# Kernel tuning notes

Measured on AMD Instinct MI355X. Metric: run time of the kernel, lower is better.

Reference implementation:

```python
import jax, jax.numpy as jnp
import numpy as np
from jax import lax

WINDOW_SIZE = 11
SIGMA = 1.5
CHANNELS = 3
C1 = 0.01 ** 2
C2 = 0.03 ** 2


def _create_window():
    coords = jnp.arange(WINDOW_SIZE, dtype=jnp.float32) - WINDOW_SIZE // 2
    g = jnp.exp(-coords ** 2 / (2.0 * SIGMA ** 2))
    g = g / g.sum()
    w2d = g[:, None] * g[None, :]                      # (11, 11)
    # depthwise kernel, OIHW with groups=channels -> (C, 1, k, k)
    return jnp.broadcast_to(w2d, (CHANNELS, 1, WINDOW_SIZE, WINDOW_SIZE))


def _dwconv(x, window):
    pad = WINDOW_SIZE // 2
    return lax.conv_general_dilated(
        x, window,
        window_strides=(1, 1),
        padding=[(pad, pad), (pad, pad)],
        dimension_numbers=('NCHW', 'OIHW', 'NCHW'),
        feature_group_count=CHANNELS,
    )


def setup_inputs() -> dict:
    key = jax.random.key(0)
    k1, k2 = jax.random.split(key)
    pred = jax.random.uniform(k1, (32, 3, 512, 512), dtype=jnp.float32)
    target = jax.random.uniform(k2, (32, 3, 512, 512), dtype=jnp.float32)
    return {"pred": pred, "target": target}


def reference(pred, target):
    pred = pred.astype(jnp.float32)
    target = target.astype(jnp.float32)
    window = _create_window()

    mu1 = _dwconv(pred, window)
    mu2 = _dwconv(target, window)
    mu1_sq = mu1 * mu1
    mu2_sq = mu2 * mu2
    mu1_mu2 = mu1 * mu2
    sigma1_sq = _dwconv(pred * pred, window) - mu1_sq
    sigma2_sq = _dwconv(target * target, window) - mu2_sq
    sigma12 = _dwconv(pred * target, window) - mu1_mu2

    ssim_map = ((2.0 * mu1_mu2 + C1) * (2.0 * sigma12 + C2)) / (
        (mu1_sq + mu2_sq + C1) * (sigma1_sq + sigma2_sq + C2))
    return 1.0 - ssim_map.mean()
```

## Files before the change

kernel.cpp:

```cpp
#include <hip/hip_runtime.h>
#include <hip/hip_bf16.h>
#include <math.h>

#define BLOCK 256
#define IMG 512
#define CHUNK 128
#define NSTEP 9
#define RSTR 40
#define NBLOCKS 3072
#define NACC 128
#define N_TOTAL 25165824.0f

typedef float f32x4 __attribute__((ext_vector_type(4)));
typedef short s16x8 __attribute__((ext_vector_type(8)));

struct WB { unsigned short b[11]; float corr; };
union FR { unsigned int u[4]; s16x8 s; };

__device__ __forceinline__ unsigned int pk2(float a, float b) {
    union { __hip_bfloat162 h; unsigned int u; } cv;
    cv.h = __float22bfloat162_rn(make_float2(a, b));
    return cv.u;
}

__global__ __launch_bounds__(BLOCK, 5)
void ssim_stream(const float* __restrict__ pred,
                 const float* __restrict__ targ,
                 float* __restrict__ accum, WB wb) {
    __shared__ unsigned short s_w[3][16][32];
    __shared__ unsigned short s_ring[4][5][16][RSTR];

    const int tid = threadIdx.x;
    for (int e = tid; e < 3 * 512; e += BLOCK) {
        const int mat = e >> 9;
        const int m   = (e >> 5) & 15;
        const int k   = e & 31;
        int idx;
        if (mat == 0) idx = k - m - 3;
        else          idx = (k - m - (mat == 2 ? 16 : 0)) & 31;
        s_w[mat][m][k] = (idx >= 0 && idx <= 10) ? wb.b[idx] : (unsigned short)0;
    }
    __syncthreads();

    const int wave = tid >> 6;
    const int lane = tid & 63;
    const int l15  = lane & 15;
    const int quad = lane >> 4;

    const int S     = blockIdx.x * 4 + wave;
    const int plane = S >> 7;
    const int rem   = S & 127;
    const int C0    = (rem >> 2) * 16;
    const int R0    = (rem & 3) * CHUNK;

    const float* P = pred + (size_t)plane * (IMG * IMG);
    const float* T = targ + (size_t)plane * (IMG * IMG);

    FR bw;  bw.s  = *(const s16x8*)&s_w[0][l15][quad * 8];
    FR aw0; aw0.s = *(const s16x8*)&s_w[1][l15][quad * 8];
    FR aw1; aw1.s = *(const s16x8*)&s_w[2][l15][quad * 8];

    unsigned short (*ring)[16][RSTR] = s_ring[wave];

    const int  cb    = C0 - 8 + 8 * quad;
    const bool colok = (cb >= 0) && (cb <= IMG - 8);
    const float corr = wb.corr;
    const float C1v = 0.0001f, C2v = 0.0009f;
    const f32x4 z = {0.f, 0.f, 0.f, 0.f};
    float lsum = 0.f;

    float xc[8], yc[8];
    {
        const int gr = R0 - 5 + l15;
        const bool ok = colok && (gr >= 0) && (gr < IMG);
        if (ok) {
            const float* rp = P + ((size_t)gr << 9) + cb;
            const float* tp = T + ((size_t)gr << 9) + cb;
            float4 a0 = *(const float4*)rp, a1 = *(const float4*)(rp + 4);
            float4 b0 = *(const float4*)tp, b1 = *(const float4*)(tp + 4);
            xc[0]=a0.x; xc[1]=a0.y; xc[2]=a0.z; xc[3]=a0.w;
            xc[4]=a1.x; xc[5]=a1.y; xc[6]=a1.z; xc[7]=a1.w;
            yc[0]=b0.x; yc[1]=b0.y; yc[2]=b0.z; yc[3]=b0.w;
            yc[4]=b1.x; yc[5]=b1.y; yc[6]=b1.z; yc[7]=b1.w;
        } else {
#pragma unroll
            for (int i = 0; i < 8; ++i) { xc[i] = 0.f; yc[i] = 0.f; }
        }
    }

    for (int s = 0; s < NSTEP; ++s) {
        float xn[8], yn[8];
        const bool have_next = (s + 1 < NSTEP);
        if (have_next) {
            const int gr = R0 - 5 + 16 * (s + 1) + l15;
            const bool ok = colok && (gr >= 0) && (gr < IMG);
            if (ok) {
                const float* rp = P + ((size_t)gr << 9) + cb;
                const float* tp = T + ((size_t)gr << 9) + cb;
                float4 a0 = *(const float4*)rp, a1 = *(const float4*)(rp + 4);
                float4 b0 = *(const float4*)tp, b1 = *(const float4*)(tp + 4);
                xn[0]=a0.x; xn[1]=a0.y; xn[2]=a0.z; xn[3]=a0.w;
                xn[4]=a1.x; xn[5]=a1.y; xn[6]=a1.z; xn[7]=a1.w;
                yn[0]=b0.x; yn[1]=b0.y; yn[2]=b0.z; yn[3]=b0.w;
                yn[4]=b1.x; yn[5]=b1.y; yn[6]=b1.z; yn[7]=b1.w;
            } else {
#pragma unroll
                for (int i = 0; i < 8; ++i) { xn[i] = 0.f; yn[i] = 0.f; }
            }
        } else {
#pragma unroll
            for (int i = 0; i < 8; ++i) { xn[i] = 0.f; yn[i] = 0.f; }
        }

        FR ax, ay, axx, ayy, axy;
#pragma unroll
        for (int p = 0; p < 4; ++p) {
            const float xa = xc[2*p], xb = xc[2*p+1];
            const float ya = yc[2*p], yb = yc[2*p+1];
            ax.u[p]  = pk2(xa, xb);
            ay.u[p]  = pk2(ya, yb);
            axx.u[p] = pk2(xa * xa, xb * xb);
            ayy.u[p] = pk2(ya * ya, yb * yb);
            axy.u[p] = pk2(xa * ya, xb * yb);
        }
        f32x4 d0 = __builtin_amdgcn_mfma_f32_16x16x32_bf16(ax.s,  bw.s, z, 0, 0, 0);
        f32x4 d1 = __builtin_amdgcn_mfma_f32_16x16x32_bf16(ay.s,  bw.s, z, 0, 0, 0);
        f32x4 d2 = __builtin_amdgcn_mfma_f32_16x16x32_bf16(axx.s, bw.s, z, 0, 0, 0);
        f32x4 d3 = __builtin_amdgcn_mfma_f32_16x16x32_bf16(ayy.s, bw.s, z, 0, 0, 0);
        f32x4 d4 = __builtin_amdgcn_mfma_f32_16x16x32_bf16(axy.s, bw.s, z, 0, 0, 0);

        const int pb = (16 * s + 4 * quad) & 31;
        *(uint2*)&ring[0][l15][pb] = make_uint2(pk2(d0[0], d0[1]), pk2(d0[2], d0[3]));
        *(uint2*)&ring[1][l15][pb] = make_uint2(pk2(d1[0], d1[1]), pk2(d1[2], d1[3]));
        *(uint2*)&ring[2][l15][pb] = make_uint2(pk2(d2[0], d2[1]), pk2(d2[2], d2[3]));
        *(uint2*)&ring[3][l15][pb] = make_uint2(pk2(d3[0], d3[1]), pk2(d3[2], d3[3]));
        *(uint2*)&ring[4][l15][pb] = make_uint2(pk2(d4[0], d4[1]), pk2(d4[2], d4[3]));

        if (s >= 1) {
            const int t = s - 1;
            const FR aw = (t & 1) ? aw1 : aw0;
            f32x4 acc[5];
#pragma unroll
            for (int q = 0; q < 5; ++q) {
                FR b; b.s = *(const s16x8*)&ring[q][l15][quad * 8];
                acc[q] = __builtin_amdgcn_mfma_f32_16x16x32_bf16(aw.s, b.s, z, 0, 0, 0);
            }
#pragma unroll
            for (int i = 0; i < 4; ++i) {
                const float mu1 = acc[0][i] * corr;
                const float mu2 = acc[1][i] * corr;
                const float exx = acc[2][i] * corr;
                const float eyy = acc[3][i] * corr;
                const float exy = acc[4][i] * corr;
                const float mu1s = mu1 * mu1;
                const float mu2s = mu2 * mu2;
                const float mu12 = mu1 * mu2;
                const float sg1  = exx - mu1s;
                const float sg2  = eyy - mu2s;
                const float sg12 = exy - mu12;
                const float num  = fmaf(2.f, mu12, C1v) * fmaf(2.f, sg12, C2v);
                const float den  = (mu1s + mu2s + C1v) * (sg1 + sg2 + C2v);
                lsum = fmaf(num, __builtin_amdgcn_rcpf(den), lsum);
            }
        }

#pragma unroll
        for (int i = 0; i < 8; ++i) { xc[i] = xn[i]; yc[i] = yn[i]; }
    }

#pragma unroll
    for (int off = 32; off > 0; off >>= 1) lsum += __shfl_down(lsum, off, 64);
    if (lane == 0) atomicAdd(&accum[S & (NACC - 1)], lsum);
}

__global__ void ssim_finalize(const float* __restrict__ accum, float* __restrict__ out) {
    const int l = threadIdx.x;
    float v = accum[l] + accum[l + 64];
#pragma unroll
    for (int off = 32; off > 0; off >>= 1) v += __shfl_down(v, off, 64);
    if (l == 0) out[0] = 1.0f - v * (1.0f / N_TOTAL);
}

extern "C" void kernel_launch(void* const* d_in, const int* in_sizes, int n_in,
                              void* d_out, int out_size, void* d_ws, size_t ws_size,
                              hipStream_t stream) {
    const float* pred = (const float*)d_in[0];
    const float* targ = (const float*)d_in[1];
    float* out = (float*)d_out;
    float* ws  = (float*)d_ws;

    WB wb;
    {
        double gg[11], sum = 0.0;
        for (int k = 0; k < 11; ++k) {
            const double d = (double)(k - 5);
            gg[k] = exp(-d * d / 4.5);
            sum += gg[k];
        }
        double sbf = 0.0;
        for (int k = 0; k < 11; ++k) {
            union { float f; unsigned int u; } cv;
            cv.f = (float)(gg[k] / sum);
            const unsigned int r = (cv.u + 0x7fffu + ((cv.u >> 16) & 1u)) >> 16;
            wb.b[k] = (unsigned short)r;
            union { float f; unsigned int u; } bk;
            bk.u = r << 16;
            sbf += (double)bk.f;
        }
        wb.corr = (float)(1.0 / (sbf * sbf));
    }

    hipMemsetAsync(ws, 0, NACC * sizeof(float), stream);
    ssim_stream<<<NBLOCKS, BLOCK, 0, stream>>>(pred, targ, ws, wb);
    ssim_finalize<<<1, 64, 0, stream>>>(ws, out);
}
```

Measured before the change: 273.5 us.

## Share horizontal halo across waves via block-wide bf16 staging tile

Each block now cooperatively loads an 80-column strip of both images, converts the five products to bf16 in shared memory, and lets four waves each compute a 16-column output slice from it. This removes the redundant halo loads and conversions each wave previously did on its own 32-column window. In exchange it adds two block barriers per row step, more shared memory, and lowers the occupancy hint from 5 to 3 blocks.

```diff
diff --git a/kernel.cpp b/kernel.cpp
--- a/kernel.cpp
+++ b/kernel.cpp
@@ -4,8 +4,7 @@
 
 #define BLOCK 256
 #define IMG 512
-#define CHUNK 128
-#define NSTEP 9
+#define SW 84
 #define RSTR 40
 #define NBLOCKS 3072
 #define NACC 128
@@ -23,12 +22,22 @@
     return cv.u;
 }
 
-__global__ __launch_bounds__(BLOCK, 5)
-void ssim_stream(const float* __restrict__ pred,
-                 const float* __restrict__ targ,
-                 float* __restrict__ accum, WB wb) {
+__device__ __forceinline__ void stage5(unsigned short (*sq)[16][SW],
+                                       int r, int i, float4 xv, float4 yv) {
+    *(uint2*)&sq[0][r][4*i] = make_uint2(pk2(xv.x,xv.y), pk2(xv.z,xv.w));
+    *(uint2*)&sq[1][r][4*i] = make_uint2(pk2(yv.x,yv.y), pk2(yv.z,yv.w));
+    *(uint2*)&sq[2][r][4*i] = make_uint2(pk2(xv.x*xv.x,xv.y*xv.y), pk2(xv.z*xv.z,xv.w*xv.w));
+    *(uint2*)&sq[3][r][4*i] = make_uint2(pk2(yv.x*yv.x,yv.y*yv.y), pk2(yv.z*yv.z,yv.w*yv.w));
+    *(uint2*)&sq[4][r][4*i] = make_uint2(pk2(xv.x*yv.x,xv.y*yv.y), pk2(xv.z*yv.z,xv.w*yv.w));
+}
+
+__global__ __launch_bounds__(BLOCK, 3)
+void ssim_tiled(const float* __restrict__ pred,
+                const float* __restrict__ targ,
+                float* __restrict__ accum, WB wb) {
     __shared__ unsigned short s_w[3][16][32];
-    __shared__ unsigned short s_ring[4][5][16][RSTR];
+    __shared__ unsigned short s_q[5][16][SW];
+    __shared__ unsigned short s_ring[5][64][RSTR];
 
     const int tid = threadIdx.x;
     for (int e = tid; e < 3 * 512; e += BLOCK) {
@@ -40,101 +49,97 @@
         else          idx = (k - m - (mat == 2 ? 16 : 0)) & 31;
         s_w[mat][m][k] = (idx >= 0 && idx <= 10) ? wb.b[idx] : (unsigned short)0;
     }
-    __syncthreads();
-
-    const int wave = tid >> 6;
+
+    const int bx    = blockIdx.x;
+    const int plane = bx >> 5;
+    const int rem   = bx & 31;
+    const int tx    = rem >> 2;
+    const int ry    = rem & 3;
+    const int C0    = tx * 64;
+    const int R0    = ry * 128;
+
+    const float* P = pred + (size_t)plane * (IMG * IMG);
+    const float* T = targ + (size_t)plane * (IMG * IMG);
+
+    const int w    = tid >> 6;
     const int lane = tid & 63;
     const int l15  = lane & 15;
     const int quad = lane >> 4;
 
-    const int S     = blockIdx.x * 4 + wave;
-    const int plane = S >> 7;
-    const int rem   = S & 127;
-    const int C0    = (rem >> 2) * 16;
-    const int R0    = (rem & 3) * CHUNK;
-
-    const float* P = pred + (size_t)plane * (IMG * IMG);
-    const float* T = targ + (size_t)plane * (IMG * IMG);
-
-    FR bw;  bw.s  = *(const s16x8*)&s_w[0][l15][quad * 8];
-    FR aw0; aw0.s = *(const s16x8*)&s_w[1][l15][quad * 8];
-    FR aw1; aw1.s = *(const s16x8*)&s_w[2][l15][quad * 8];
-
-    unsigned short (*ring)[16][RSTR] = s_ring[wave];
-
-    const int  cb    = C0 - 8 + 8 * quad;
-    const bool colok = (cb >= 0) && (cb <= IMG - 8);
+    const int slotA = w * 80 + lane;
+    const int rA = slotA / 20, iA = slotA % 20;
+    const int colA = C0 - 8 + 4 * iA;
+    const bool okcA = (colA >= 0) && (colA + 4 <= IMG);
+    const bool hasB = (lane < 16);
+    const int slotB = w * 80 + 64 + l15;
+    const int rB = slotB / 20, iB = slotB % 20;
+    const int colB = C0 - 8 + 4 * iB;
+    const bool okcB = (colB >= 0) && (colB + 4 <= IMG);
+
     const float corr = wb.corr;
     const float C1v = 0.0001f, C2v = 0.0009f;
     const f32x4 z = {0.f, 0.f, 0.f, 0.f};
     float lsum = 0.f;
 
-    float xc[8], yc[8];
+    float4 xA, yA, xB, yB;
     {
-        const int gr = R0 - 5 + l15;
-        const bool ok = colok && (gr >= 0) && (gr < IMG);
-        if (ok) {
-            const float* rp = P + ((size_t)gr << 9) + cb;
-            const float* tp = T + ((size_t)gr << 9) + cb;
-            float4 a0 = *(const float4*)rp, a1 = *(const float4*)(rp + 4);
-            float4 b0 = *(const float4*)tp, b1 = *(const float4*)(tp + 4);
-            xc[0]=a0.x; xc[1]=a0.y; xc[2]=a0.z; xc[3]=a0.w;
-            xc[4]=a1.x; xc[5]=a1.y; xc[6]=a1.z; xc[7]=a1.w;
-            yc[0]=b0.x; yc[1]=b0.y; yc[2]=b0.z; yc[3]=b0.w;
-            yc[4]=b1.x; yc[5]=b1.y; yc[6]=b1.z; yc[7]=b1.w;
-        } else {
-#pragma unroll
-            for (int i = 0; i < 8; ++i) { xc[i] = 0.f; yc[i] = 0.f; }
-        }
-    }
-
-    for (int s = 0; s < NSTEP; ++s) {
-        float xn[8], yn[8];
-        const bool have_next = (s + 1 < NSTEP);
-        if (have_next) {
-            const int gr = R0 - 5 + 16 * (s + 1) + l15;
-            const bool ok = colok && (gr >= 0) && (gr < IMG);
-            if (ok) {
-                const float* rp = P + ((size_t)gr << 9) + cb;
-                const float* tp = T + ((size_t)gr << 9) + cb;
-                float4 a0 = *(const float4*)rp, a1 = *(const float4*)(rp + 4);
-                float4 b0 = *(const float4*)tp, b1 = *(const float4*)(tp + 4);
-                xn[0]=a0.x; xn[1]=a0.y; xn[2]=a0.z; xn[3]=a0.w;
-                xn[4]=a1.x; xn[5]=a1.y; xn[6]=a1.z; xn[7]=a1.w;
-                yn[0]=b0.x; yn[1]=b0.y; yn[2]=b0.z; yn[3]=b0.w;
-                yn[4]=b1.x; yn[5]=b1.y; yn[6]=b1.z; yn[7]=b1.w;
-            } else {
-#pragma unroll
-                for (int i = 0; i < 8; ++i) { xn[i] = 0.f; yn[i] = 0.f; }
-            }
-        } else {
-#pragma unroll
-            for (int i = 0; i < 8; ++i) { xn[i] = 0.f; yn[i] = 0.f; }
-        }
-
-        FR ax, ay, axx, ayy, axy;
-#pragma unroll
-        for (int p = 0; p < 4; ++p) {
-            const float xa = xc[2*p], xb = xc[2*p+1];
-            const float ya = yc[2*p], yb = yc[2*p+1];
-            ax.u[p]  = pk2(xa, xb);
-            ay.u[p]  = pk2(ya, yb);
-            axx.u[p] = pk2(xa * xa, xb * xb);
-            ayy.u[p] = pk2(ya * ya, yb * yb);
-            axy.u[p] = pk2(xa * ya, xb * yb);
-        }
-        f32x4 d0 = __builtin_amdgcn_mfma_f32_16x16x32_bf16(ax.s,  bw.s, z, 0, 0, 0);
-        f32x4 d1 = __builtin_amdgcn_mfma_f32_16x16x32_bf16(ay.s,  bw.s, z, 0, 0, 0);
-        f32x4 d2 = __builtin_amdgcn_mfma_f32_16x16x32_bf16(axx.s, bw.s, z, 0, 0, 0);
-        f32x4 d3 = __builtin_amdgcn_mfma_f32_16x16x32_bf16(ayy.s, bw.s, z, 0, 0, 0);
-        f32x4 d4 = __builtin_amdgcn_mfma_f32_16x16x32_bf16(axy.s, bw.s, z, 0, 0, 0);
-
-        const int pb = (16 * s + 4 * quad) & 31;
-        *(uint2*)&ring[0][l15][pb] = make_uint2(pk2(d0[0], d0[1]), pk2(d0[2], d0[3]));
-        *(uint2*)&ring[1][l15][pb] = make_uint2(pk2(d1[0], d1[1]), pk2(d1[2], d1[3]));
-        *(uint2*)&ring[2][l15][pb] = make_uint2(pk2(d2[0], d2[1]), pk2(d2[2], d2[3]));
-        *(uint2*)&ring[3][l15][pb] = make_uint2(pk2(d3[0], d3[1]), pk2(d3[2], d3[3]));
-        *(uint2*)&ring[4][l15][pb] = make_uint2(pk2(d4[0], d4[1]), pk2(d4[2], d4[3]));
+        const int gr = R0 - 5 + rA;
+        if (okcA && gr >= 0) {
+            xA = *(const float4*)(P + ((size_t)gr << 9) + colA);
+            yA = *(const float4*)(T + ((size_t)gr << 9) + colA);
+        } else { xA = make_float4(0,0,0,0); yA = make_float4(0,0,0,0); }
+        const int grB = R0 - 5 + rB;
+        if (hasB && okcB && grB >= 0) {
+            xB = *(const float4*)(P + ((size_t)grB << 9) + colB);
+            yB = *(const float4*)(T + ((size_t)grB << 9) + colB);
+        } else { xB = make_float4(0,0,0,0); yB = make_float4(0,0,0,0); }
+    }
+    __syncthreads();
+
+    FR bw;  bw.s  = *(const s16x8*)&s_w[0][l15][quad * 8];
+    FR aw0; aw0.s = *(const s16x8*)&s_w[1][l15][quad * 8];
+    FR aw1; aw1.s = *(const s16x8*)&s_w[2][l15][quad * 8];
+
+    stage5(s_q, rA, iA, xA, yA);
+    if (hasB) stage5(s_q, rB, iB, xB, yB);
+    __syncthreads();
+
+    const int rcol = 16 * w + l15;
+
+    for (int s = 0; s < 9; ++s) {
+        float4 nxA, nyA, nxB, nyB;
+        if (s < 8) {
+            const int gr = R0 - 5 + 16 * (s + 1) + rA;
+            if (okcA && gr < IMG) {
+                nxA = *(const float4*)(P + ((size_t)gr << 9) + colA);
+                nyA = *(const float4*)(T + ((size_t)gr << 9) + colA);
+            } else { nxA = make_float4(0,0,0,0); nyA = make_float4(0,0,0,0); }
+            const int grB = R0 - 5 + 16 * (s + 1) + rB;
+            if (hasB && okcB && grB < IMG) {
+                nxB = *(const float4*)(P + ((size_t)grB << 9) + colB);
+                nyB = *(const float4*)(T + ((size_t)grB << 9) + colB);
+            } else { nxB = make_float4(0,0,0,0); nyB = make_float4(0,0,0,0); }
+        }
+
+        {
+            FR a0, a1, a2, a3, a4;
+            a0.s = *(const s16x8*)&s_q[0][l15][16*w + 8*quad];
+            a1.s = *(const s16x8*)&s_q[1][l15][16*w + 8*quad];
+            a2.s = *(const s16x8*)&s_q[2][l15][16*w + 8*quad];
+            a3.s = *(const s16x8*)&s_q[3][l15][16*w + 8*quad];
+            a4.s = *(const s16x8*)&s_q[4][l15][16*w + 8*quad];
+            f32x4 d0 = __builtin_amdgcn_mfma_f32_16x16x32_bf16(a0.s, bw.s, z, 0, 0, 0);
+            f32x4 d1 = __builtin_amdgcn_mfma_f32_16x16x32_bf16(a1.s, bw.s, z, 0, 0, 0);
+            f32x4 d2 = __builtin_amdgcn_mfma_f32_16x16x32_bf16(a2.s, bw.s, z, 0, 0, 0);
+            f32x4 d3 = __builtin_amdgcn_mfma_f32_16x16x32_bf16(a3.s, bw.s, z, 0, 0, 0);
+            f32x4 d4 = __builtin_amdgcn_mfma_f32_16x16x32_bf16(a4.s, bw.s, z, 0, 0, 0);
+            const int pb = (16 * s + 4 * quad) & 31;
+            *(uint2*)&s_ring[0][rcol][pb] = make_uint2(pk2(d0[0],d0[1]), pk2(d0[2],d0[3]));
+            *(uint2*)&s_ring[1][rcol][pb] = make_uint2(pk2(d1[0],d1[1]), pk2(d1[2],d1[3]));
+            *(uint2*)&s_ring[2][rcol][pb] = make_uint2(pk2(d2[0],d2[1]), pk2(d2[2],d2[3]));
+            *(uint2*)&s_ring[3][rcol][pb] = make_uint2(pk2(d3[0],d3[1]), pk2(d3[2],d3[3]));
+            *(uint2*)&s_ring[4][rcol][pb] = make_uint2(pk2(d4[0],d4[1]), pk2(d4[2],d4[3]));
+        }
 
         if (s >= 1) {
             const int t = s - 1;
@@ -142,7 +147,7 @@
             f32x4 acc[5];
 #pragma unroll
             for (int q = 0; q < 5; ++q) {
-                FR b; b.s = *(const s16x8*)&ring[q][l15][quad * 8];
+                FR b; b.s = *(const s16x8*)&s_ring[q][rcol][quad * 8];
                 acc[q] = __builtin_amdgcn_mfma_f32_16x16x32_bf16(aw.s, b.s, z, 0, 0, 0);
             }
 #pragma unroll
@@ -164,13 +169,18 @@
             }
         }
 
-#pragma unroll
-        for (int i = 0; i < 8; ++i) { xc[i] = xn[i]; yc[i] = yn[i]; }
+        __syncthreads();
+
+        if (s < 8) {
+            stage5(s_q, rA, iA, nxA, nyA);
+            if (hasB) stage5(s_q, rB, iB, nxB, nyB);
+            __syncthreads();
+        }
     }
 
 #pragma unroll
     for (int off = 32; off > 0; off >>= 1) lsum += __shfl_down(lsum, off, 64);
-    if (lane == 0) atomicAdd(&accum[S & (NACC - 1)], lsum);
+    if (lane == 0) atomicAdd(&accum[(bx * 4 + w) & (NACC - 1)], lsum);
 }
 
 __global__ void ssim_finalize(const float* __restrict__ accum, float* __restrict__ out) {
@@ -211,6 +221,6 @@
     }
 
     hipMemsetAsync(ws, 0, NACC * sizeof(float), stream);
-    ssim_stream<<<NBLOCKS, BLOCK, 0, stream>>>(pred, targ, ws, wb);
+    ssim_tiled<<<NBLOCKS, BLOCK, 0, stream>>>(pred, targ, ws, wb);
     ssim_finalize<<<1, 64, 0, stream>>>(ws, out);
 }
```

New measurement: 265.4 us. 1.03x faster.
